# Kernel tuning notes

Hardware: AMD Instinct MI355X
Metric: run time of the kernel (lower is better)

Reference implementation:

```python
import jax, jax.numpy as jnp
import numpy as np

N, E = 20000, 320000
IN, OUT, MID, EC, L = 128, 128, 32, 32, 1
SQRT3 = 1.7320508075688772
EPS = 1e-5


def _xavier(key, fan_in, fan_out, shape=None):
    shape = shape if shape is not None else (fan_in, fan_out)
    std = (2.0 / (fan_in + fan_out)) ** 0.5
    return jax.random.normal(key, shape, dtype=jnp.float32) * std


def layer_norm(x, w, b):
    mu = x.mean(axis=-1, keepdims=True)
    var = ((x - mu) ** 2).mean(axis=-1, keepdims=True)
    return (x - mu) * jax.lax.rsqrt(var + EPS) * w + b


def equ_layer_norm(x, w, b, lmax):
    # x: [N, (lmax+1)^2, C]; per-l RMS norm over (m, channel); l=0 mean-centered + bias.
    segs = []
    for l in range(lmax + 1):
        f = x[:, l * l:(l + 1) * (l + 1), :]
        if l == 0:
            f = f - f.mean(axis=-1, keepdims=True)
        norm = jnp.mean(f * f, axis=(1, 2), keepdims=True)
        f = f * jax.lax.rsqrt(norm + EPS) * w[l]
        if l == 0:
            f = f + b
        segs.append(f)
    return jnp.concatenate(segs, axis=1)


def gate_3j(x, w, lmax, channel):
    # x: [N, (lmax+1)^2, C]; w: [C, C*(lmax+1)] (jax in,out layout)
    after = x[:, 0, :] @ w
    type0 = after[:, :channel]
    mult = jax.nn.sigmoid(after[:, channel:])  # [N, lmax*C]
    parts = [jax.nn.silu(type0)[:, None, :]]
    for l in range(1, lmax + 1):
        parts.append(x[:, l * l:(l + 1) * (l + 1), :] * mult[:, None, (l - 1) * channel:l * channel])
    return jnp.concatenate(parts, axis=1)


def setup_inputs() -> dict:
    key = jax.random.key(0)
    ks = jax.random.split(key, 24)
    inp = {
        'feats': jax.random.normal(ks[0], (N, IN), dtype=jnp.float32),
        'equ': jax.random.normal(ks[1], (N, (L + 1) ** 2, EC), dtype=jnp.float32),
        'points': jax.random.normal(ks[2], (N, 3), dtype=jnp.float32),
        'neighbors': jax.random.randint(ks[3], (2, E), 0, N, dtype=jnp.int64) if jax.config.jax_enable_x64 else jax.random.randint(ks[3], (2, E), 0, N, dtype=jnp.int32),
        # params (jax Linear layout: [in, out])
        'ln1_w': jnp.ones((IN,), jnp.float32), 'ln1_b': jnp.zeros((IN,), jnp.float32),
        'eqn1_w': jnp.ones((L + 1, EC), jnp.float32), 'eqn1_b': jnp.zeros((EC,), jnp.float32),
        'inv_fc_w': _xavier(ks[4], IN, MID), 'inv_fc_b': jnp.zeros((MID,), jnp.float32),
        'equ_fc_w': _xavier(ks[5], EC, MID),
        'fc_l0_w': _xavier(ks[6], 2 * MID, MID), 'fc_l0_b': jnp.zeros((MID,), jnp.float32),
        'equ_fc_2_w': _xavier(ks[7], MID, EC),
        'inv_fc_1_w': _xavier(ks[8], 3 * MID, OUT), 'inv_fc_1_b': jnp.zeros((OUT,), jnp.float32),
        'ffn_ln_w': jnp.ones((OUT,), jnp.float32), 'ffn_ln_b': jnp.zeros((OUT,), jnp.float32),
        'ffn_w1': _xavier(ks[9], OUT, OUT), 'ffn_b1': jnp.zeros((OUT,), jnp.float32),
        'ffn_w2': _xavier(ks[10], OUT, OUT), 'ffn_b2': jnp.zeros((OUT,), jnp.float32),
        'eqn2_w': jnp.ones((L + 1, EC), jnp.float32), 'eqn2_b': jnp.zeros((EC,), jnp.float32),
        'fe1_w': _xavier(ks[11], EC, MID),
        'gate_w': _xavier(ks[12], MID, MID * (L + 1)),
        'fe2_w': _xavier(ks[13], MID, EC),
    }
    return inp


def reference(feats, equ, points, neighbors, ln1_w, ln1_b, eqn1_w, eqn1_b,
              inv_fc_w, inv_fc_b, equ_fc_w, fc_l0_w, fc_l0_b, equ_fc_2_w,
              inv_fc_1_w, inv_fc_1_b, ffn_ln_w, ffn_ln_b, ffn_w1, ffn_b1,
              ffn_w2, ffn_b2, eqn2_w, eqn2_b, fe1_w, gate_w, fe2_w):
    n = feats.shape[0]
    feats = layer_norm(feats, ln1_w, ln1_b)
    equ = equ_layer_norm(equ, eqn1_w, eqn1_b, L)
    feats1 = feats @ inv_fc_w + inv_fc_b              # [N, MID]
    equ1 = equ @ equ_fc_w                              # [N, 4, MID]
    src, dst = neighbors[0], neighbors[1]
    s_equ, t_equ = equ1[src], equ1[dst]                # [E, 4, MID]
    s_feats, t_feats = feats1[src], feats1[dst]        # [E, MID]
    vec = points[src] - points[dst]                    # [E, 3]
    # e3nn spherical harmonics l=0..1, normalize=False, 'component': [1, sqrt(3)*v]
    sh = jnp.concatenate([jnp.ones((vec.shape[0], 1), vec.dtype), SQRT3 * vec], axis=1)  # [E, 4]
    dot1 = jnp.sum(s_equ * t_equ, axis=1)              # [E, MID]
    dot2 = jnp.sum(s_equ * sh[:, :, None], axis=1)     # [E, MID]
    equ_l0 = jax.nn.silu(jnp.concatenate([dot1, dot2], axis=1) @ fc_l0_w + fc_l0_b)
    equ_message = jnp.concatenate([equ_l0[:, None, :], s_equ[:, 1:, :]], axis=1)  # [E, 4, MID]
    equ_message = equ_message @ equ_fc_2_w             # [E, 4, EC]
    inv_message = jax.nn.silu(jnp.concatenate([s_feats, t_feats, equ_l0], axis=-1) @ inv_fc_1_w + inv_fc_1_b)  # [E, OUT]
    nb_cnt = (jnp.max(inv_message, axis=-1, keepdims=True) > 0.0).astype(feats.dtype)  # [E, 1]
    neighbors_new = jnp.ones((n, 1), feats.dtype).at[dst].add(nb_cnt)
    inv_new = jnp.zeros((n, OUT), feats.dtype).at[dst].add(inv_message) + feats  # shortcut1 = Identity
    inv_new = inv_new / neighbors_new
    equ_new = jnp.zeros((n, (L + 1) ** 2, EC), feats.dtype).at[dst].add(equ_message) + equ  # shortcut2 = Identity
    equ_new = equ_new / neighbors_new[:, :, None]
    # ffn_inv
    h = layer_norm(inv_new, ffn_ln_w, ffn_ln_b)
    h = jax.nn.relu(h @ ffn_w1 + ffn_b1) @ ffn_w2 + ffn_b2
    inv_new = h + inv_new
    # ffn_equ
    g = equ_layer_norm(equ_new, eqn2_w, eqn2_b, L) @ fe1_w
    g = gate_3j(g, gate_w, L, MID) @ fe2_w
    equ_new = g + equ_new
    return inv_new, equ_new
```

## Files before the change

### kernel.cpp

```cpp
#include <hip/hip_runtime.h>
#include <math.h>

#define EPS 1e-5f
#define SQRT3F 1.7320508075688772f

__device__ __forceinline__ float wsum64(float x) {
#pragma unroll
    for (int o = 32; o > 0; o >>= 1) x += __shfl_xor(x, o, 64);
    return x;
}
__device__ __forceinline__ float hsum32(float x) {
#pragma unroll
    for (int o = 16; o > 0; o >>= 1) x += __shfl_xor(x, o, 64);
    return x;
}
__device__ __forceinline__ float sigm(float x) { return 1.f / (1.f + __expf(-x)); }
__device__ __forceinline__ float siluf(float x) { return x * sigm(x); }

__global__ __launch_bounds__(256) void node_pre(
    int N,
    const float* __restrict__ feats, const float* __restrict__ equ,
    const float* __restrict__ ln1_w, const float* __restrict__ ln1_b,
    const float* __restrict__ eqn1_w, const float* __restrict__ eqn1_b,
    const float* __restrict__ inv_fc_w, const float* __restrict__ inv_fc_b,
    const float* __restrict__ equ_fc_w, const float* __restrict__ Winv,
    float* __restrict__ feats_ln, float* __restrict__ equ_ln,
    float* __restrict__ equ1t, float* __restrict__ PsP, float* __restrict__ PtP)
{
    __shared__ float fl_s[4][128];
    __shared__ float el_s[4][128];
    __shared__ float f1_s[4][32];
    const int w = threadIdx.x >> 6;
    const int lane = threadIdx.x & 63;
    const int n = blockIdx.x * 4 + w;
    const bool act = n < N;
    const int c = lane & 31;
    const int half = lane >> 5;

    float x0 = 0.f, x1 = 0.f;
    if (act) { x0 = feats[n * 128 + lane]; x1 = feats[n * 128 + 64 + lane]; }
    float s  = wsum64(x0 + x1);
    float sq = wsum64(x0 * x0 + x1 * x1);
    float mu = s * (1.f / 128.f);
    float var = sq * (1.f / 128.f) - mu * mu;
    float rs = rsqrtf(var + EPS);
    float y0 = (x0 - mu) * rs * ln1_w[lane] + ln1_b[lane];
    float y1 = (x1 - mu) * rs * ln1_w[64 + lane] + ln1_b[64 + lane];
    if (act) { feats_ln[n * 128 + lane] = y0; feats_ln[n * 128 + 64 + lane] = y1; }
    fl_s[w][lane] = y0; fl_s[w][64 + lane] = y1;

    float a = 0.f, b = 0.f;
    if (act) { a = equ[n * 128 + lane]; b = equ[n * 128 + 64 + lane]; }
    float a0 = (half == 0) ? a : 0.f;
    float m0 = wsum64(a0) * (1.f / 32.f);
    float f0 = a0 - m0;
    float n0 = wsum64((half == 0) ? f0 * f0 : 0.f) * (1.f / 32.f);
    float rs0 = rsqrtf(n0 + EPS);
    float sq1 = ((half == 1) ? a * a : 0.f) + b * b;
    float n1 = wsum64(sq1) * (1.f / 96.f);
    float rs1 = rsqrtf(n1 + EPS);
    float w1c = eqn1_w[32 + c];
    float ea = (half == 0) ? (f0 * rs0 * eqn1_w[c] + eqn1_b[c]) : (a * rs1 * w1c);
    float eb = b * rs1 * w1c;
    if (act) { equ_ln[n * 128 + lane] = ea; equ_ln[n * 128 + 64 + lane] = eb; }
    el_s[w][lane] = ea; el_s[w][64 + lane] = eb;

    __syncthreads();

    {
        float acc = 0.f;
#pragma unroll 8
        for (int k = 0; k < 64; k++) {
            int kk = half * 64 + k;
            acc += fl_s[w][kk] * inv_fc_w[kk * 32 + c];
        }
        acc += __shfl_xor(acc, 32);
        if (half == 0) f1_s[w][c] = acc + inv_fc_b[c];
    }
    if (act) {
        float acc = 0.f, acc2 = 0.f;
#pragma unroll 8
        for (int k = 0; k < 32; k++) {
            float wv = equ_fc_w[k * 32 + c];
            acc  += el_s[w][half * 32 + k] * wv;
            acc2 += el_s[w][(half + 2) * 32 + k] * wv;
        }
        equ1t[n * 128 + c * 4 + half]     = acc;
        equ1t[n * 128 + c * 4 + half + 2] = acc2;
    }
    __syncthreads();
    if (!act) return;

    {
        const int jj = c;
        float4 aPs = {0.f, 0.f, 0.f, 0.f};
        float4 aPt = {0.f, 0.f, 0.f, 0.f};
#pragma unroll 4
        for (int k = 0; k < 16; k++) {
            int kk = half * 16 + k;
            float x = f1_s[w][kk];
            float4 w4 = *(const float4*)&Winv[kk * 128 + jj * 4];
            float4 v4 = *(const float4*)&Winv[(32 + kk) * 128 + jj * 4];
            aPs.x += x * w4.x; aPs.y += x * w4.y; aPs.z += x * w4.z; aPs.w += x * w4.w;
            aPt.x += x * v4.x; aPt.y += x * v4.y; aPt.z += x * v4.z; aPt.w += x * v4.w;
        }
        aPs.x += __shfl_xor(aPs.x, 32); aPs.y += __shfl_xor(aPs.y, 32);
        aPs.z += __shfl_xor(aPs.z, 32); aPs.w += __shfl_xor(aPs.w, 32);
        aPt.x += __shfl_xor(aPt.x, 32); aPt.y += __shfl_xor(aPt.y, 32);
        aPt.z += __shfl_xor(aPt.z, 32); aPt.w += __shfl_xor(aPt.w, 32);
        if (half == 0) {
            const float* ps = (const float*)&aPs;
            const float* pt = (const float*)&aPt;
#pragma unroll
            for (int i = 0; i < 4; i++) {
                int m = jj * 4 + i;
                PsP[n * 128 + (m & 31) * 4 + (m >> 5)] = ps[i];
                PtP[n * 128 + (m & 31) * 4 + (m >> 5)] = pt[i];
            }
        }
    }
}

__global__ __launch_bounds__(256) void csr_hist(int E, const int* __restrict__ nb,
                                                int* __restrict__ deg)
{
    int i = blockIdx.x * 256 + threadIdx.x;
    if (i < E) atomicAdd(&deg[nb[E + i]], 1);
}

__global__ __launch_bounds__(1024) void csr_scan(int N, const int* __restrict__ deg,
                                                 int* __restrict__ row_start,
                                                 int* __restrict__ cursor)
{
    __shared__ int part[1024];
    const int t = threadIdx.x;
    const int per = (N + 1023) / 1024;
    const int base = t * per;
    int s = 0;
    for (int i = 0; i < per; i++) { int idx = base + i; if (idx < N) s += deg[idx]; }
    part[t] = s;
    __syncthreads();
    for (int off = 1; off < 1024; off <<= 1) {
        int v = (t >= off) ? part[t - off] : 0;
        __syncthreads();
        part[t] += v;
        __syncthreads();
    }
    int run = (t > 0) ? part[t - 1] : 0;
    for (int i = 0; i < per; i++) {
        int idx = base + i;
        if (idx < N) { row_start[idx] = run; cursor[idx] = run; run += deg[idx]; }
    }
}

__global__ __launch_bounds__(256) void csr_scatter(int E, const int* __restrict__ nb,
                                                   int* __restrict__ cursor,
                                                   int* __restrict__ csr_src)
{
    int i = blockIdx.x * 256 + threadIdx.x;
    if (i < E) {
        int d = nb[E + i];
        int s = nb[i];
        int pos = atomicAdd(&cursor[d], 1);
        csr_src[pos] = s;
    }
}

__global__ __launch_bounds__(256) void edge_agg(
    int N,
    const int* __restrict__ row_start, const int* __restrict__ deg_arr,
    const int* __restrict__ csr_src,
    const float* __restrict__ points, const float* __restrict__ equ1t,
    const float* __restrict__ PsP, const float* __restrict__ PtP,
    const float* __restrict__ feats_ln, const float* __restrict__ equ_ln,
    const float* __restrict__ Wl0g, const float* __restrict__ bl0g,
    const float* __restrict__ We2g, const float* __restrict__ Winvg,
    const float* __restrict__ binvg,
    float* __restrict__ out_inv, float* __restrict__ out_equ)
{
    __shared__ float WeP[32 * 128];
    __shared__ float Wl0P[16 * 128];
    __shared__ float We2P[8 * 128];
    __shared__ float BinvP[128];
    __shared__ float bl0s[32];
    __shared__ float scr[8][128];

    for (int idx = threadIdx.x; idx < 4096; idx += 256) {
        int k = idx >> 7, r = idx & 127, cc = r >> 2, j = r & 3;
        WeP[idx] = Winvg[(64 + k) * 128 + j * 32 + cc];
    }
    for (int idx = threadIdx.x; idx < 2048; idx += 256) {
        int g = idx >> 7, r = idx & 127, cc = r >> 2, i = r & 3;
        Wl0P[idx] = Wl0g[(g * 4 + i) * 32 + cc];
    }
    for (int idx = threadIdx.x; idx < 1024; idx += 256) {
        int g = idx >> 7, r = idx & 127, cc = r >> 2, i = r & 3;
        We2P[idx] = We2g[(g * 4 + i) * 32 + cc];
    }
    if (threadIdx.x < 128) BinvP[threadIdx.x] = binvg[(threadIdx.x & 3) * 32 + (threadIdx.x >> 2)];
    if (threadIdx.x < 32) bl0s[threadIdx.x] = bl0g[threadIdx.x];
    __syncthreads();

    const int grp = threadIdx.x >> 5;
    const int c = threadIdx.x & 31;
    const int halfsel = grp & 1;
    const int n = blockIdx.x * 8 + grp;
    if (n >= N) return;

    const int start = row_start[n];
    const int len = deg_arr[n];
    float4 te4 = *(const float4*)&equ1t[n * 128 + c * 4];
    float4 pt4 = *(const float4*)&PtP[n * 128 + c * 4];
    const float pdx = points[n * 3 + 0], pdy = points[n * 3 + 1], pdz = points[n * 3 + 2];
    float4 base = *(const float4*)&BinvP[c * 4];
    base.x += pt4.x; base.y += pt4.y; base.z += pt4.z; base.w += pt4.w;

    float4 acc = {0.f, 0.f, 0.f, 0.f};
    float4 aer = {0.f, 0.f, 0.f, 0.f};
    int cnt = 0;
    int i = 0;

    for (; i + 2 <= len; i += 2) {
        const int s0 = csr_src[start + i];
        const int s1 = csr_src[start + i + 1];
        float4 a0 = *(const float4*)&equ1t[s0 * 128 + c * 4];
        float4 a1 = *(const float4*)&equ1t[s1 * 128 + c * 4];
        float4 p0 = *(const float4*)&PsP[s0 * 128 + c * 4];
        float4 p1 = *(const float4*)&PsP[s1 * 128 + c * 4];
        float dx0 = SQRT3F * (points[s0 * 3 + 0] - pdx);
        float dy0 = SQRT3F * (points[s0 * 3 + 1] - pdy);
        float dz0 = SQRT3F * (points[s0 * 3 + 2] - pdz);
        float dx1 = SQRT3F * (points[s1 * 3 + 0] - pdx);
        float dy1 = SQRT3F * (points[s1 * 3 + 1] - pdy);
        float dz1 = SQRT3F * (points[s1 * 3 + 2] - pdz);
        scr[grp][c]      = a0.x * te4.x + a0.y * te4.y + a0.z * te4.z + a0.w * te4.w;
        scr[grp][32 + c] = a0.x + a0.y * dx0 + a0.z * dy0 + a0.w * dz0;
        scr[grp][64 + c] = a1.x * te4.x + a1.y * te4.y + a1.z * te4.z + a1.w * te4.w;
        scr[grp][96 + c] = a1.x + a1.y * dx1 + a1.z * dy1 + a1.w * dz1;

        float e0acc = bl0s[c], e1acc = bl0s[c];
#pragma unroll
        for (int g = 0; g < 16; g++) {
            float4 w4 = *(const float4*)&Wl0P[g * 128 + c * 4];
            float4 d0 = *(const float4*)&scr[grp][g * 4];
            float4 d1 = *(const float4*)&scr[grp][64 + g * 4];
            e0acc += d0.x * w4.x + d0.y * w4.y + d0.z * w4.z + d0.w * w4.w;
            e1acc += d1.x * w4.x + d1.y * w4.y + d1.z * w4.z + d1.w * w4.w;
        }
        float el0_0 = siluf(e0acc);
        float el0_1 = siluf(e1acc);
        aer.x += el0_0 + el0_1;
        aer.y += a0.y + a1.y; aer.z += a0.z + a1.z; aer.w += a0.w + a1.w;
        scr[grp][c] = el0_0;
        scr[grp][32 + c] = el0_1;

        float4 m0 = base, m1 = base;
        m0.x += p0.x; m0.y += p0.y; m0.z += p0.z; m0.w += p0.w;
        m1.x += p1.x; m1.y += p1.y; m1.z += p1.z; m1.w += p1.w;
#pragma unroll
        for (int g = 0; g < 8; g++) {
            float4 x0 = *(const float4*)&scr[grp][g * 4];
            float4 x1 = *(const float4*)&scr[grp][32 + g * 4];
            const float* xp0 = (const float*)&x0;
            const float* xp1 = (const float*)&x1;
#pragma unroll
            for (int t = 0; t < 4; t++) {
                float4 w4 = *(const float4*)&WeP[(g * 4 + t) * 128 + c * 4];
                float v0 = xp0[t], v1 = xp1[t];
                m0.x += v0 * w4.x; m0.y += v0 * w4.y; m0.z += v0 * w4.z; m0.w += v0 * w4.w;
                m1.x += v1 * w4.x; m1.y += v1 * w4.y; m1.z += v1 * w4.z; m1.w += v1 * w4.w;
            }
        }
        m0.x = siluf(m0.x); m0.y = siluf(m0.y); m0.z = siluf(m0.z); m0.w = siluf(m0.w);
        m1.x = siluf(m1.x); m1.y = siluf(m1.y); m1.z = siluf(m1.z); m1.w = siluf(m1.w);
        acc.x += m0.x + m1.x; acc.y += m0.y + m1.y;
        acc.z += m0.z + m1.z; acc.w += m0.w + m1.w;
        float mx0 = fmaxf(fmaxf(m0.x, m0.y), fmaxf(m0.z, m0.w));
        float mx1 = fmaxf(fmaxf(m1.x, m1.y), fmaxf(m1.z, m1.w));
        unsigned long long b0 = __ballot(mx0 > 0.f);
        unsigned long long b1 = __ballot(mx1 > 0.f);
        cnt += ((unsigned int)(b0 >> (halfsel * 32)) != 0u);
        cnt += ((unsigned int)(b1 >> (halfsel * 32)) != 0u);
    }
    for (; i < len; i++) {
        const int s0 = csr_src[start + i];
        float4 a0 = *(const float4*)&equ1t[s0 * 128 + c * 4];
        float4 p0 = *(const float4*)&PsP[s0 * 128 + c * 4];
        float dx0 = SQRT3F * (points[s0 * 3 + 0] - pdx);
        float dy0 = SQRT3F * (points[s0 * 3 + 1] - pdy);
        float dz0 = SQRT3F * (points[s0 * 3 + 2] - pdz);
        scr[grp][c]      = a0.x * te4.x + a0.y * te4.y + a0.z * te4.z + a0.w * te4.w;
        scr[grp][32 + c] = a0.x + a0.y * dx0 + a0.z * dy0 + a0.w * dz0;
        float e0acc = bl0s[c];
#pragma unroll
        for (int g = 0; g < 16; g++) {
            float4 w4 = *(const float4*)&Wl0P[g * 128 + c * 4];
            float4 d0 = *(const float4*)&scr[grp][g * 4];
            e0acc += d0.x * w4.x + d0.y * w4.y + d0.z * w4.z + d0.w * w4.w;
        }
        float el0_0 = siluf(e0acc);
        aer.x += el0_0; aer.y += a0.y; aer.z += a0.z; aer.w += a0.w;
        scr[grp][c] = el0_0;
        float4 m0 = base;
        m0.x += p0.x; m0.y += p0.y; m0.z += p0.z; m0.w += p0.w;
#pragma unroll
        for (int g = 0; g < 8; g++) {
            float4 x0 = *(const float4*)&scr[grp][g * 4];
            const float* xp0 = (const float*)&x0;
#pragma unroll
            for (int t = 0; t < 4; t++) {
                float4 w4 = *(const float4*)&WeP[(g * 4 + t) * 128 + c * 4];
                float v0 = xp0[t];
                m0.x += v0 * w4.x; m0.y += v0 * w4.y; m0.z += v0 * w4.z; m0.w += v0 * w4.w;
            }
        }
        m0.x = siluf(m0.x); m0.y = siluf(m0.y); m0.z = siluf(m0.z); m0.w = siluf(m0.w);
        acc.x += m0.x; acc.y += m0.y; acc.z += m0.z; acc.w += m0.w;
        float mx0 = fmaxf(fmaxf(m0.x, m0.y), fmaxf(m0.z, m0.w));
        unsigned long long b0 = __ballot(mx0 > 0.f);
        cnt += ((unsigned int)(b0 >> (halfsel * 32)) != 0u);
    }

    const float inv_nbn = 1.f / (1.f + (float)cnt);
    out_inv[n * 128 + c]      = (acc.x + feats_ln[n * 128 + c])      * inv_nbn;
    out_inv[n * 128 + 32 + c] = (acc.y + feats_ln[n * 128 + 32 + c]) * inv_nbn;
    out_inv[n * 128 + 64 + c] = (acc.z + feats_ln[n * 128 + 64 + c]) * inv_nbn;
    out_inv[n * 128 + 96 + c] = (acc.w + feats_ln[n * 128 + 96 + c]) * inv_nbn;

    *(float4*)&scr[grp][c * 4] = aer;
    float4 eo = {0.f, 0.f, 0.f, 0.f};
#pragma unroll
    for (int g = 0; g < 8; g++) {
        float4 w4 = *(const float4*)&We2P[g * 128 + c * 4];
        const float* wp = (const float*)&w4;
#pragma unroll
        for (int t = 0; t < 4; t++) {
            float4 a4 = *(const float4*)&scr[grp][(g * 4 + t) * 4];
            float wv = wp[t];
            eo.x += a4.x * wv; eo.y += a4.y * wv; eo.z += a4.z * wv; eo.w += a4.w * wv;
        }
    }
    out_equ[n * 128 + c]      = (eo.x + equ_ln[n * 128 + c])      * inv_nbn;
    out_equ[n * 128 + 32 + c] = (eo.y + equ_ln[n * 128 + 32 + c]) * inv_nbn;
    out_equ[n * 128 + 64 + c] = (eo.z + equ_ln[n * 128 + 64 + c]) * inv_nbn;
    out_equ[n * 128 + 96 + c] = (eo.w + equ_ln[n * 128 + 96 + c]) * inv_nbn;
}

__global__ __launch_bounds__(256) void node_post(
    int N,
    const float* __restrict__ ffn_ln_w, const float* __restrict__ ffn_ln_b,
    const float* __restrict__ W1g, const float* __restrict__ b1g,
    const float* __restrict__ W2g, const float* __restrict__ b2g,
    const float* __restrict__ eqn2_w, const float* __restrict__ eqn2_b,
    const float* __restrict__ fe1, const float* __restrict__ gate_w,
    const float* __restrict__ fe2,
    float* __restrict__ io_inv, float* __restrict__ io_equ)
{
    __shared__ float ht[128 * 36];
    __shared__ float es[8][128];
    __shared__ float gs[8][128];
    __shared__ float fe1P[8 * 128];
    __shared__ float fe2P[8 * 128];
    __shared__ float gatePa[8 * 128];
    __shared__ float gatePb[8 * 128];

    for (int idx = threadIdx.x; idx < 1024; idx += 256) {
        int g = idx >> 7, r = idx & 127, cc = r >> 2, i = r & 3;
        fe1P[idx]   = fe1[(g * 4 + i) * 32 + cc];
        fe2P[idx]   = fe2[(g * 4 + i) * 32 + cc];
        gatePa[idx] = gate_w[(g * 4 + i) * 64 + cc];
        gatePb[idx] = gate_w[(g * 4 + i) * 64 + 32 + cc];
    }
    __syncthreads();

    const int grp = threadIdx.x >> 5;
    const int c = threadIdx.x & 31;

    for (int q = 0; q < 4; q++) {
        const int nd = grp * 4 + q;
        const int n = blockIdx.x * 32 + nd;
        if (n >= N) break;

        float eq0 = io_equ[n * 128 + c];
        float eq1 = io_equ[n * 128 + 32 + c];
        float eq2 = io_equ[n * 128 + 64 + c];
        float eq3 = io_equ[n * 128 + 96 + c];
        float m0 = hsum32(eq0) * (1.f / 32.f);
        float f0 = eq0 - m0;
        float n0 = hsum32(f0 * f0) * (1.f / 32.f);
        float rs0 = rsqrtf(n0 + EPS);
        float n1 = hsum32(eq1 * eq1 + eq2 * eq2 + eq3 * eq3) * (1.f / 96.f);
        float rs1 = rsqrtf(n1 + EPS);
        float w1c = eqn2_w[32 + c];
        float4 ev;
        ev.x = f0 * rs0 * eqn2_w[c] + eqn2_b[c];
        ev.y = eq1 * rs1 * w1c;
        ev.z = eq2 * rs1 * w1c;
        ev.w = eq3 * rs1 * w1c;
        *(float4*)&es[grp][c * 4] = ev;

        float4 g4 = {0.f, 0.f, 0.f, 0.f};
#pragma unroll
        for (int g = 0; g < 8; g++) {
            float4 w4 = *(const float4*)&fe1P[g * 128 + c * 4];
            const float* wp = (const float*)&w4;
#pragma unroll
            for (int t = 0; t < 4; t++) {
                float4 a4 = *(const float4*)&es[grp][(g * 4 + t) * 4];
                float wv = wp[t];
                g4.x += a4.x * wv; g4.y += a4.y * wv; g4.z += a4.z * wv; g4.w += a4.w * wv;
            }
        }
        *(float4*)&gs[grp][c * 4] = g4;

        float aftA = 0.f, aftB = 0.f;
#pragma unroll
        for (int g = 0; g < 8; g++) {
            float4 wa4 = *(const float4*)&gatePa[g * 128 + c * 4];
            float4 wb4 = *(const float4*)&gatePb[g * 128 + c * 4];
            const float* wap = (const float*)&wa4;
            const float* wbp = (const float*)&wb4;
#pragma unroll
            for (int t = 0; t < 4; t++) {
                float g0 = gs[grp][(g * 4 + t) * 4];
                aftA += g0 * wap[t];
                aftB += g0 * wbp[t];
            }
        }
        float mult = sigm(aftB);
        float4 G;
        G.x = siluf(aftA);
        G.y = g4.y * mult; G.z = g4.z * mult; G.w = g4.w * mult;
        *(float4*)&es[grp][c * 4] = G;

        float4 oo = {0.f, 0.f, 0.f, 0.f};
#pragma unroll
        for (int g = 0; g < 8; g++) {
            float4 w4 = *(const float4*)&fe2P[g * 128 + c * 4];
            const float* wp = (const float*)&w4;
#pragma unroll
            for (int t = 0; t < 4; t++) {
                float4 a4 = *(const float4*)&es[grp][(g * 4 + t) * 4];
                float wv = wp[t];
                oo.x += a4.x * wv; oo.y += a4.y * wv; oo.z += a4.z * wv; oo.w += a4.w * wv;
            }
        }
        io_equ[n * 128 + c]      = oo.x + eq0;
        io_equ[n * 128 + 32 + c] = oo.y + eq1;
        io_equ[n * 128 + 64 + c] = oo.z + eq2;
        io_equ[n * 128 + 96 + c] = oo.w + eq3;

        float ip0 = io_inv[n * 128 + c];
        float ip1 = io_inv[n * 128 + 32 + c];
        float ip2 = io_inv[n * 128 + 64 + c];
        float ip3 = io_inv[n * 128 + 96 + c];
        float sm = hsum32(ip0 + ip1 + ip2 + ip3) * (1.f / 128.f);
        float sv = hsum32(ip0 * ip0 + ip1 * ip1 + ip2 * ip2 + ip3 * ip3) * (1.f / 128.f) - sm * sm;
        float rsv = rsqrtf(sv + EPS);
        ht[c * 36 + nd]         = (ip0 - sm) * rsv * ffn_ln_w[c]      + ffn_ln_b[c];
        ht[(32 + c) * 36 + nd]  = (ip1 - sm) * rsv * ffn_ln_w[32 + c] + ffn_ln_b[32 + c];
        ht[(64 + c) * 36 + nd]  = (ip2 - sm) * rsv * ffn_ln_w[64 + c] + ffn_ln_b[64 + c];
        ht[(96 + c) * 36 + nd]  = (ip3 - sm) * rsv * ffn_ln_w[96 + c] + ffn_ln_b[96 + c];
    }

    const int wid = threadIdx.x >> 6;
    const int half = (threadIdx.x >> 5) & 1;
    const int ndbase = wid * 8;
    const int nbase = blockIdx.x * 32 + ndbase;

    float4 acc8[8];
#pragma unroll
    for (int j = 0; j < 8; j++) acc8[j] = make_float4(0.f, 0.f, 0.f, 0.f);
    for (int k = 0; k < 64; k++) {
        const int kk = half * 64 + k;
        float4 w4 = *(const float4*)&W1g[kk * 128 + c * 4];
        float4 xA = *(const float4*)&ht[kk * 36 + ndbase];
        float4 xB = *(const float4*)&ht[kk * 36 + ndbase + 4];
        const float* xa = (const float*)&xA;
        const float* xb = (const float*)&xB;
#pragma unroll
        for (int j = 0; j < 4; j++) {
            float v = xa[j];
            acc8[j].x += v * w4.x; acc8[j].y += v * w4.y; acc8[j].z += v * w4.z; acc8[j].w += v * w4.w;
            float u = xb[j];
            acc8[4 + j].x += u * w4.x; acc8[4 + j].y += u * w4.y; acc8[4 + j].z += u * w4.z; acc8[4 + j].w += u * w4.w;
        }
    }
#pragma unroll
    for (int j = 0; j < 8; j++) {
        acc8[j].x += __shfl_xor(acc8[j].x, 32); acc8[j].y += __shfl_xor(acc8[j].y, 32);
        acc8[j].z += __shfl_xor(acc8[j].z, 32); acc8[j].w += __shfl_xor(acc8[j].w, 32);
    }
    if (half == 0) {
        float4 b4 = *(const float4*)&b1g[c * 4];
#pragma unroll
        for (int j = 0; j < 8; j++) {
            float r0 = fmaxf(acc8[j].x + b4.x, 0.f);
            float r1 = fmaxf(acc8[j].y + b4.y, 0.f);
            float r2 = fmaxf(acc8[j].z + b4.z, 0.f);
            float r3 = fmaxf(acc8[j].w + b4.w, 0.f);
            ht[(4 * c + 0) * 36 + ndbase + j] = r0;
            ht[(4 * c + 1) * 36 + ndbase + j] = r1;
            ht[(4 * c + 2) * 36 + ndbase + j] = r2;
            ht[(4 * c + 3) * 36 + ndbase + j] = r3;
        }
    }
#pragma unroll
    for (int j = 0; j < 8; j++) acc8[j] = make_float4(0.f, 0.f, 0.f, 0.f);
    for (int k = 0; k < 64; k++) {
        const int kk = half * 64 + k;
        float4 w4 = *(const float4*)&W2g[kk * 128 + c * 4];
        float4 xA = *(const float4*)&ht[kk * 36 + ndbase];
        float4 xB = *(const float4*)&ht[kk * 36 + ndbase + 4];
        const float* xa = (const float*)&xA;
        const float* xb = (const float*)&xB;
#pragma unroll
        for (int j = 0; j < 4; j++) {
            float v = xa[j];
            acc8[j].x += v * w4.x; acc8[j].y += v * w4.y; acc8[j].z += v * w4.z; acc8[j].w += v * w4.w;
            float u = xb[j];
            acc8[4 + j].x += u * w4.x; acc8[4 + j].y += u * w4.y; acc8[4 + j].z += u * w4.z; acc8[4 + j].w += u * w4.w;
        }
    }
#pragma unroll
    for (int j = 0; j < 8; j++) {
        acc8[j].x += __shfl_xor(acc8[j].x, 32); acc8[j].y += __shfl_xor(acc8[j].y, 32);
        acc8[j].z += __shfl_xor(acc8[j].z, 32); acc8[j].w += __shfl_xor(acc8[j].w, 32);
    }
    if (half == 0) {
        float4 b4 = *(const float4*)&b2g[c * 4];
#pragma unroll
        for (int j = 0; j < 8; j++) {
            const int n = nbase + j;
            if (n < N) {
                float4 ipre = *(const float4*)&io_inv[n * 128 + c * 4];
                float4 o;
                o.x = acc8[j].x + b4.x + ipre.x;
                o.y = acc8[j].y + b4.y + ipre.y;
                o.z = acc8[j].z + b4.z + ipre.z;
                o.w = acc8[j].w + b4.w + ipre.w;
                *(float4*)&io_inv[n * 128 + c * 4] = o;
            }
        }
    }
}

extern "C" void kernel_launch(void* const* d_in, const int* in_sizes, int n_in,
                              void* d_out, int out_size, void* d_ws, size_t ws_size,
                              hipStream_t stream)
{
    const float* feats     = (const float*)d_in[0];
    const float* equ       = (const float*)d_in[1];
    const float* points    = (const float*)d_in[2];
    const int*   neighbors = (const int*)d_in[3];
    const float* ln1_w     = (const float*)d_in[4];
    const float* ln1_b     = (const float*)d_in[5];
    const float* eqn1_w    = (const float*)d_in[6];
    const float* eqn1_b    = (const float*)d_in[7];
    const float* inv_fc_w  = (const float*)d_in[8];
    const float* inv_fc_b  = (const float*)d_in[9];
    const float* equ_fc_w  = (const float*)d_in[10];
    const float* fc_l0_w   = (const float*)d_in[11];
    const float* fc_l0_b   = (const float*)d_in[12];
    const float* equ_fc_2_w= (const float*)d_in[13];
    const float* inv_fc_1_w= (const float*)d_in[14];
    const float* inv_fc_1_b= (const float*)d_in[15];
    const float* ffn_ln_w  = (const float*)d_in[16];
    const float* ffn_ln_b  = (const float*)d_in[17];
    const float* ffn_w1    = (const float*)d_in[18];
    const float* ffn_b1    = (const float*)d_in[19];
    const float* ffn_w2    = (const float*)d_in[20];
    const float* ffn_b2    = (const float*)d_in[21];
    const float* eqn2_w    = (const float*)d_in[22];
    const float* eqn2_b    = (const float*)d_in[23];
    const float* fe1_w     = (const float*)d_in[24];
    const float* gate_w    = (const float*)d_in[25];
    const float* fe2_w     = (const float*)d_in[26];

    const int N = in_sizes[0] / 128;
    const int E = in_sizes[3] / 2;

    float* ws = (float*)d_ws;
    float* feats_ln = ws;
    float* equ_ln   = feats_ln + (size_t)N * 128;
    float* equ1t    = equ_ln   + (size_t)N * 128;
    float* PsP      = equ1t    + (size_t)N * 128;
    float* PtP      = PsP      + (size_t)N * 128;
    int* deg        = (int*)(PtP + (size_t)N * 128);
    int* row_start  = deg + N;
    int* cursor     = row_start + N;
    int* csr_src    = cursor + N;

    hipMemsetAsync(deg, 0, (size_t)N * sizeof(int), stream);

    node_pre<<<(N + 3) / 4, 256, 0, stream>>>(
        N, feats, equ, ln1_w, ln1_b, eqn1_w, eqn1_b,
        inv_fc_w, inv_fc_b, equ_fc_w, inv_fc_1_w,
        feats_ln, equ_ln, equ1t, PsP, PtP);

    csr_hist<<<(E + 255) / 256, 256, 0, stream>>>(E, neighbors, deg);
    csr_scan<<<1, 1024, 0, stream>>>(N, deg, row_start, cursor);
    csr_scatter<<<(E + 255) / 256, 256, 0, stream>>>(E, neighbors, cursor, csr_src);

    float* out_inv = (float*)d_out;
    float* out_equ = out_inv + (size_t)N * 128;

    edge_agg<<<(N + 7) / 8, 256, 0, stream>>>(
        N, row_start, deg, csr_src,
        points, equ1t, PsP, PtP, feats_ln, equ_ln,
        fc_l0_w, fc_l0_b, equ_fc_2_w, inv_fc_1_w, inv_fc_1_b,
        out_inv, out_equ);

    node_post<<<(N + 31) / 32, 256, 0, stream>>>(
        N, ffn_ln_w, ffn_ln_b, ffn_w1, ffn_b1, ffn_w2, ffn_b2,
        eqn2_w, eqn2_b, fe1_w, gate_w, fe2_w,
        out_inv, out_equ);
}
```

Measured before the change: 512.5 us.

## Fuse CSR kernels, sort nodes by degree, and move equ FFN into edge_agg

```diff
diff --git a/kernel.cpp b/kernel.cpp
--- a/kernel.cpp
+++ b/kernel.cpp
@@ -17,16 +17,24 @@
 __device__ __forceinline__ float sigm(float x) { return 1.f / (1.f + __expf(-x)); }
 __device__ __forceinline__ float siluf(float x) { return x * sigm(x); }
 
-__global__ __launch_bounds__(256) void node_pre(
-    int N,
+__global__ __launch_bounds__(256) void pre_and_hist(
+    int N, int E, int nb_pre,
     const float* __restrict__ feats, const float* __restrict__ equ,
+    const int* __restrict__ nbrs, const float* __restrict__ points,
     const float* __restrict__ ln1_w, const float* __restrict__ ln1_b,
     const float* __restrict__ eqn1_w, const float* __restrict__ eqn1_b,
     const float* __restrict__ inv_fc_w, const float* __restrict__ inv_fc_b,
     const float* __restrict__ equ_fc_w, const float* __restrict__ Winv,
     float* __restrict__ feats_ln, float* __restrict__ equ_ln,
-    float* __restrict__ equ1t, float* __restrict__ PsP, float* __restrict__ PtP)
+    float* __restrict__ equ1t, float* __restrict__ PsP, float* __restrict__ PtP,
+    float* __restrict__ points4, int* __restrict__ deg)
 {
+    if (blockIdx.x >= nb_pre) {
+        int i = (blockIdx.x - nb_pre) * 256 + threadIdx.x;
+        if (i < E) atomicAdd(&deg[nbrs[E + i]], 1);
+        return;
+    }
+
     __shared__ float fl_s[4][128];
     __shared__ float el_s[4][128];
     __shared__ float f1_s[4][32];
@@ -36,6 +44,13 @@
     const bool act = n < N;
     const int c = lane & 31;
     const int half = lane >> 5;
+
+    if (act && lane == 0) {
+        float4 p;
+        p.x = points[n * 3 + 0]; p.y = points[n * 3 + 1];
+        p.z = points[n * 3 + 2]; p.w = 0.f;
+        *(float4*)&points4[n * 4] = p;
+    }
 
     float x0 = 0.f, x1 = 0.f;
     if (act) { x0 = feats[n * 128 + lane]; x1 = feats[n * 128 + 64 + lane]; }
@@ -121,23 +136,43 @@
     }
 }
 
-__global__ __launch_bounds__(256) void csr_hist(int E, const int* __restrict__ nb,
-                                                int* __restrict__ deg)
-{
-    int i = blockIdx.x * 256 + threadIdx.x;
-    if (i < E) atomicAdd(&deg[nb[E + i]], 1);
-}
-
-__global__ __launch_bounds__(1024) void csr_scan(int N, const int* __restrict__ deg,
-                                                 int* __restrict__ row_start,
-                                                 int* __restrict__ cursor)
+__global__ __launch_bounds__(1024) void csr_scan(
+    int N, const int* __restrict__ deg,
+    int* __restrict__ row_start, int* __restrict__ cursor,
+    int* __restrict__ bucket_start, int* __restrict__ bucket_cursor,
+    const float* __restrict__ fe1, const float* __restrict__ fe2,
+    const float* __restrict__ gate_w, const float* __restrict__ We2,
+    float* __restrict__ fe1P, float* __restrict__ fe2P,
+    float* __restrict__ gatePa, float* __restrict__ gatePb,
+    float* __restrict__ We2P)
 {
     __shared__ int part[1024];
+    __shared__ int hist[64];
     const int t = threadIdx.x;
+
+    if (t < 1024) {
+        int g = t >> 7, r = t & 127, cc = r >> 2, i = r & 3;
+        fe1P[t]   = fe1[(g * 4 + i) * 32 + cc];
+        fe2P[t]   = fe2[(g * 4 + i) * 32 + cc];
+        gatePa[t] = gate_w[(g * 4 + i) * 64 + cc];
+        gatePb[t] = gate_w[(g * 4 + i) * 64 + 32 + cc];
+        We2P[t]   = We2[(g * 4 + i) * 32 + cc];
+    }
+
+    if (t < 64) hist[t] = 0;
+    __syncthreads();
+
     const int per = (N + 1023) / 1024;
     const int base = t * per;
     int s = 0;
-    for (int i = 0; i < per; i++) { int idx = base + i; if (idx < N) s += deg[idx]; }
+    for (int i = 0; i < per; i++) {
+        int idx = base + i;
+        if (idx < N) {
+            int d = deg[idx];
+            s += d;
+            atomicAdd(&hist[d < 63 ? d : 63], 1);
+        }
+    }
     part[t] = s;
     __syncthreads();
     for (int off = 1; off < 1024; off <<= 1) {
@@ -151,36 +186,57 @@
         int idx = base + i;
         if (idx < N) { row_start[idx] = run; cursor[idx] = run; run += deg[idx]; }
     }
-}
-
-__global__ __launch_bounds__(256) void csr_scatter(int E, const int* __restrict__ nb,
-                                                   int* __restrict__ cursor,
-                                                   int* __restrict__ csr_src)
+    if (t == 0) {
+        int acc = 0;
+        for (int b = 0; b < 64; b++) {
+            bucket_start[b] = acc;
+            bucket_cursor[b] = acc;
+            acc += hist[b];
+        }
+    }
+}
+
+__global__ __launch_bounds__(256) void scatter_all(
+    int E, int N, int nbE,
+    const int* __restrict__ nb, int* __restrict__ cursor, int* __restrict__ csr_src,
+    const int* __restrict__ deg, int* __restrict__ bucket_cursor, int* __restrict__ perm)
 {
-    int i = blockIdx.x * 256 + threadIdx.x;
-    if (i < E) {
-        int d = nb[E + i];
-        int s = nb[i];
-        int pos = atomicAdd(&cursor[d], 1);
-        csr_src[pos] = s;
-    }
-}
-
-__global__ __launch_bounds__(256) void edge_agg(
+    if (blockIdx.x < nbE) {
+        int i = blockIdx.x * 256 + threadIdx.x;
+        if (i < E) {
+            int d = nb[E + i];
+            int s = nb[i];
+            int pos = atomicAdd(&cursor[d], 1);
+            csr_src[pos] = s;
+        }
+    } else {
+        int i = (blockIdx.x - nbE) * 256 + threadIdx.x;
+        if (i < N) {
+            int d = deg[i]; if (d > 63) d = 63;
+            int pos = atomicAdd(&bucket_cursor[d], 1);
+            perm[pos] = i;
+        }
+    }
+}
+
+__global__ __launch_bounds__(256, 5) void edge_agg(
     int N,
+    const int* __restrict__ perm,
     const int* __restrict__ row_start, const int* __restrict__ deg_arr,
     const int* __restrict__ csr_src,
-    const float* __restrict__ points, const float* __restrict__ equ1t,
+    const float* __restrict__ points4, const float* __restrict__ equ1t,
     const float* __restrict__ PsP, const float* __restrict__ PtP,
     const float* __restrict__ feats_ln, const float* __restrict__ equ_ln,
     const float* __restrict__ Wl0g, const float* __restrict__ bl0g,
-    const float* __restrict__ We2g, const float* __restrict__ Winvg,
-    const float* __restrict__ binvg,
+    const float* __restrict__ Winvg, const float* __restrict__ binvg,
+    const float* __restrict__ We2P, const float* __restrict__ fe1P,
+    const float* __restrict__ fe2P, const float* __restrict__ gatePa,
+    const float* __restrict__ gatePb,
+    const float* __restrict__ eqn2_w, const float* __restrict__ eqn2_b,
     float* __restrict__ out_inv, float* __restrict__ out_equ)
 {
     __shared__ float WeP[32 * 128];
     __shared__ float Wl0P[16 * 128];
-    __shared__ float We2P[8 * 128];
     __shared__ float BinvP[128];
     __shared__ float bl0s[32];
     __shared__ float scr[8][128];
@@ -193,10 +249,6 @@
         int g = idx >> 7, r = idx & 127, cc = r >> 2, i = r & 3;
         Wl0P[idx] = Wl0g[(g * 4 + i) * 32 + cc];
     }
-    for (int idx = threadIdx.x; idx < 1024; idx += 256) {
-        int g = idx >> 7, r = idx & 127, cc = r >> 2, i = r & 3;
-        We2P[idx] = We2g[(g * 4 + i) * 32 + cc];
-    }
     if (threadIdx.x < 128) BinvP[threadIdx.x] = binvg[(threadIdx.x & 3) * 32 + (threadIdx.x >> 2)];
     if (threadIdx.x < 32) bl0s[threadIdx.x] = bl0g[threadIdx.x];
     __syncthreads();
@@ -204,14 +256,15 @@
     const int grp = threadIdx.x >> 5;
     const int c = threadIdx.x & 31;
     const int halfsel = grp & 1;
-    const int n = blockIdx.x * 8 + grp;
-    if (n >= N) return;
+    const int gid = blockIdx.x * 8 + grp;
+    if (gid >= N) return;
+    const int n = perm[gid];
 
     const int start = row_start[n];
     const int len = deg_arr[n];
     float4 te4 = *(const float4*)&equ1t[n * 128 + c * 4];
     float4 pt4 = *(const float4*)&PtP[n * 128 + c * 4];
-    const float pdx = points[n * 3 + 0], pdy = points[n * 3 + 1], pdz = points[n * 3 + 2];
+    float4 pd4 = *(const float4*)&points4[n * 4];
     float4 base = *(const float4*)&BinvP[c * 4];
     base.x += pt4.x; base.y += pt4.y; base.z += pt4.z; base.w += pt4.w;
 
@@ -227,12 +280,14 @@
         float4 a1 = *(const float4*)&equ1t[s1 * 128 + c * 4];
         float4 p0 = *(const float4*)&PsP[s0 * 128 + c * 4];
         float4 p1 = *(const float4*)&PsP[s1 * 128 + c * 4];
-        float dx0 = SQRT3F * (points[s0 * 3 + 0] - pdx);
-        float dy0 = SQRT3F * (points[s0 * 3 + 1] - pdy);
-        float dz0 = SQRT3F * (points[s0 * 3 + 2] - pdz);
-        float dx1 = SQRT3F * (points[s1 * 3 + 0] - pdx);
-        float dy1 = SQRT3F * (points[s1 * 3 + 1] - pdy);
-        float dz1 = SQRT3F * (points[s1 * 3 + 2] - pdz);
+        float4 q0 = *(const float4*)&points4[s0 * 4];
+        float4 q1 = *(const float4*)&points4[s1 * 4];
+        float dx0 = SQRT3F * (q0.x - pd4.x);
+        float dy0 = SQRT3F * (q0.y - pd4.y);
+        float dz0 = SQRT3F * (q0.z - pd4.z);
+        float dx1 = SQRT3F * (q1.x - pd4.x);
+        float dy1 = SQRT3F * (q1.y - pd4.y);
+        float dz1 = SQRT3F * (q1.z - pd4.z);
         scr[grp][c]      = a0.x * te4.x + a0.y * te4.y + a0.z * te4.z + a0.w * te4.w;
         scr[grp][32 + c] = a0.x + a0.y * dx0 + a0.z * dy0 + a0.w * dz0;
         scr[grp][64 + c] = a1.x * te4.x + a1.y * te4.y + a1.z * te4.z + a1.w * te4.w;
@@ -286,9 +341,10 @@
         const int s0 = csr_src[start + i];
         float4 a0 = *(const float4*)&equ1t[s0 * 128 + c * 4];
         float4 p0 = *(const float4*)&PsP[s0 * 128 + c * 4];
-        float dx0 = SQRT3F * (points[s0 * 3 + 0] - pdx);
-        float dy0 = SQRT3F * (points[s0 * 3 + 1] - pdy);
-        float dz0 = SQRT3F * (points[s0 * 3 + 2] - pdz);
+        float4 q0 = *(const float4*)&points4[s0 * 4];
+        float dx0 = SQRT3F * (q0.x - pd4.x);
+        float dy0 = SQRT3F * (q0.y - pd4.y);
+        float dz0 = SQRT3F * (q0.z - pd4.z);
         scr[grp][c]      = a0.x * te4.x + a0.y * te4.y + a0.z * te4.z + a0.w * te4.w;
         scr[grp][32 + c] = a0.x + a0.y * dx0 + a0.z * dy0 + a0.w * dz0;
         float e0acc = bl0s[c];
@@ -340,10 +396,71 @@
             eo.x += a4.x * wv; eo.y += a4.y * wv; eo.z += a4.z * wv; eo.w += a4.w * wv;
         }
     }
-    out_equ[n * 128 + c]      = (eo.x + equ_ln[n * 128 + c])      * inv_nbn;
-    out_equ[n * 128 + 32 + c] = (eo.y + equ_ln[n * 128 + 32 + c]) * inv_nbn;
-    out_equ[n * 128 + 64 + c] = (eo.z + equ_ln[n * 128 + 64 + c]) * inv_nbn;
-    out_equ[n * 128 + 96 + c] = (eo.w + equ_ln[n * 128 + 96 + c]) * inv_nbn;
+    float4 en;
+    en.x = (eo.x + equ_ln[n * 128 + c])      * inv_nbn;
+    en.y = (eo.y + equ_ln[n * 128 + 32 + c]) * inv_nbn;
+    en.z = (eo.z + equ_ln[n * 128 + 64 + c]) * inv_nbn;
+    en.w = (eo.w + equ_ln[n * 128 + 96 + c]) * inv_nbn;
+
+    float m0e = hsum32(en.x) * (1.f / 32.f);
+    float f0 = en.x - m0e;
+    float n0 = hsum32(f0 * f0) * (1.f / 32.f);
+    float rs0 = rsqrtf(n0 + EPS);
+    float n1 = hsum32(en.y * en.y + en.z * en.z + en.w * en.w) * (1.f / 96.f);
+    float rs1 = rsqrtf(n1 + EPS);
+    float w1c = eqn2_w[32 + c];
+    float4 ev;
+    ev.x = f0 * rs0 * eqn2_w[c] + eqn2_b[c];
+    ev.y = en.y * rs1 * w1c;
+    ev.z = en.z * rs1 * w1c;
+    ev.w = en.w * rs1 * w1c;
+    *(float4*)&scr[grp][c * 4] = ev;
+
+    float4 g4 = {0.f, 0.f, 0.f, 0.f};
+#pragma unroll
+    for (int g = 0; g < 8; g++) {
+        float4 w4 = *(const float4*)&fe1P[g * 128 + c * 4];
+        const float* wp = (const float*)&w4;
+#pragma unroll
+        for (int t = 0; t < 4; t++) {
+            float4 a4 = *(const float4*)&scr[grp][(g * 4 + t) * 4];
+            float wv = wp[t];
+            g4.x += a4.x * wv; g4.y += a4.y * wv; g4.z += a4.z * wv; g4.w += a4.w * wv;
+        }
+    }
+    scr[grp][c] = g4.x;
+
+    float aftA = 0.f, aftB = 0.f;
+#pragma unroll
+    for (int g = 0; g < 8; g++) {
+        float4 x4 = *(const float4*)&scr[grp][g * 4];
+        float4 wa4 = *(const float4*)&gatePa[g * 128 + c * 4];
+        float4 wb4 = *(const float4*)&gatePb[g * 128 + c * 4];
+        aftA += x4.x * wa4.x + x4.y * wa4.y + x4.z * wa4.z + x4.w * wa4.w;
+        aftB += x4.x * wb4.x + x4.y * wb4.y + x4.z * wb4.z + x4.w * wb4.w;
+    }
+    float mult = sigm(aftB);
+    float4 G;
+    G.x = siluf(aftA);
+    G.y = g4.y * mult; G.z = g4.z * mult; G.w = g4.w * mult;
+    *(float4*)&scr[grp][c * 4] = G;
+
+    float4 oo = {0.f, 0.f, 0.f, 0.f};
+#pragma unroll
+    for (int g = 0; g < 8; g++) {
+        float4 w4 = *(const float4*)&fe2P[g * 128 + c * 4];
+        const float* wp = (const float*)&w4;
+#pragma unroll
+        for (int t = 0; t < 4; t++) {
+            float4 a4 = *(const float4*)&scr[grp][(g * 4 + t) * 4];
+            float wv = wp[t];
+            oo.x += a4.x * wv; oo.y += a4.y * wv; oo.z += a4.z * wv; oo.w += a4.w * wv;
+        }
+    }
+    out_equ[n * 128 + c]      = oo.x + en.x;
+    out_equ[n * 128 + 32 + c] = oo.y + en.y;
+    out_equ[n * 128 + 64 + c] = oo.z + en.z;
+    out_equ[n * 128 + 96 + c] = oo.w + en.w;
 }
 
 __global__ __launch_bounds__(256) void node_post(
@@ -351,28 +468,9 @@
     const float* __restrict__ ffn_ln_w, const float* __restrict__ ffn_ln_b,
     const float* __restrict__ W1g, const float* __restrict__ b1g,
     const float* __restrict__ W2g, const float* __restrict__ b2g,
-    const float* __restrict__ eqn2_w, const float* __restrict__ eqn2_b,
-    const float* __restrict__ fe1, const float* __restrict__ gate_w,
-    const float* __restrict__ fe2,
-    float* __restrict__ io_inv, float* __restrict__ io_equ)
+    float* __restrict__ io_inv)
 {
     __shared__ float ht[128 * 36];
-    __shared__ float es[8][128];
-    __shared__ float gs[8][128];
-    __shared__ float fe1P[8 * 128];
-    __shared__ float fe2P[8 * 128];
-    __shared__ float gatePa[8 * 128];
-    __shared__ float gatePb[8 * 128];
-
-    for (int idx = threadIdx.x; idx < 1024; idx += 256) {
-        int g = idx >> 7, r = idx & 127, cc = r >> 2, i = r & 3;
-        fe1P[idx]   = fe1[(g * 4 + i) * 32 + cc];
-        fe2P[idx]   = fe2[(g * 4 + i) * 32 + cc];
-        gatePa[idx] = gate_w[(g * 4 + i) * 64 + cc];
-        gatePb[idx] = gate_w[(g * 4 + i) * 64 + 32 + cc];
-    }
-    __syncthreads();
-
     const int grp = threadIdx.x >> 5;
     const int c = threadIdx.x & 31;
 
@@ -380,76 +478,6 @@
         const int nd = grp * 4 + q;
         const int n = blockIdx.x * 32 + nd;
         if (n >= N) break;
-
-        float eq0 = io_equ[n * 128 + c];
-        float eq1 = io_equ[n * 128 + 32 + c];
-        float eq2 = io_equ[n * 128 + 64 + c];
-        float eq3 = io_equ[n * 128 + 96 + c];
-        float m0 = hsum32(eq0) * (1.f / 32.f);
-        float f0 = eq0 - m0;
-        float n0 = hsum32(f0 * f0) * (1.f / 32.f);
-        float rs0 = rsqrtf(n0 + EPS);
-        float n1 = hsum32(eq1 * eq1 + eq2 * eq2 + eq3 * eq3) * (1.f / 96.f);
-        float rs1 = rsqrtf(n1 + EPS);
-        float w1c = eqn2_w[32 + c];
-        float4 ev;
-        ev.x = f0 * rs0 * eqn2_w[c] + eqn2_b[c];
-        ev.y = eq1 * rs1 * w1c;
-        ev.z = eq2 * rs1 * w1c;
-        ev.w = eq3 * rs1 * w1c;
-        *(float4*)&es[grp][c * 4] = ev;
-
-        float4 g4 = {0.f, 0.f, 0.f, 0.f};
-#pragma unroll
-        for (int g = 0; g < 8; g++) {
-            float4 w4 = *(const float4*)&fe1P[g * 128 + c * 4];
-            const float* wp = (const float*)&w4;
-#pragma unroll
-            for (int t = 0; t < 4; t++) {
-                float4 a4 = *(const float4*)&es[grp][(g * 4 + t) * 4];
-                float wv = wp[t];
-                g4.x += a4.x * wv; g4.y += a4.y * wv; g4.z += a4.z * wv; g4.w += a4.w * wv;
-            }
-        }
-        *(float4*)&gs[grp][c * 4] = g4;
-
-        float aftA = 0.f, aftB = 0.f;
-#pragma unroll
-        for (int g = 0; g < 8; g++) {
-            float4 wa4 = *(const float4*)&gatePa[g * 128 + c * 4];
-            float4 wb4 = *(const float4*)&gatePb[g * 128 + c * 4];
-            const float* wap = (const float*)&wa4;
-            const float* wbp = (const float*)&wb4;
-#pragma unroll
-            for (int t = 0; t < 4; t++) {
-                float g0 = gs[grp][(g * 4 + t) * 4];
-                aftA += g0 * wap[t];
-                aftB += g0 * wbp[t];
-            }
-        }
-        float mult = sigm(aftB);
-        float4 G;
-        G.x = siluf(aftA);
-        G.y = g4.y * mult; G.z = g4.z * mult; G.w = g4.w * mult;
-        *(float4*)&es[grp][c * 4] = G;
-
-        float4 oo = {0.f, 0.f, 0.f, 0.f};
-#pragma unroll
-        for (int g = 0; g < 8; g++) {
-            float4 w4 = *(const float4*)&fe2P[g * 128 + c * 4];
-            const float* wp = (const float*)&w4;
-#pragma unroll
-            for (int t = 0; t < 4; t++) {
-                float4 a4 = *(const float4*)&es[grp][(g * 4 + t) * 4];
-                float wv = wp[t];
-                oo.x += a4.x * wv; oo.y += a4.y * wv; oo.z += a4.z * wv; oo.w += a4.w * wv;
-            }
-        }
-        io_equ[n * 128 + c]      = oo.x + eq0;
-        io_equ[n * 128 + 32 + c] = oo.y + eq1;
-        io_equ[n * 128 + 64 + c] = oo.z + eq2;
-        io_equ[n * 128 + 96 + c] = oo.w + eq3;
-
         float ip0 = io_inv[n * 128 + c];
         float ip1 = io_inv[n * 128 + 32 + c];
         float ip2 = io_inv[n * 128 + 64 + c];
@@ -495,14 +523,10 @@
         float4 b4 = *(const float4*)&b1g[c * 4];
 #pragma unroll
         for (int j = 0; j < 8; j++) {
-            float r0 = fmaxf(acc8[j].x + b4.x, 0.f);
-            float r1 = fmaxf(acc8[j].y + b4.y, 0.f);
-            float r2 = fmaxf(acc8[j].z + b4.z, 0.f);
-            float r3 = fmaxf(acc8[j].w + b4.w, 0.f);
-            ht[(4 * c + 0) * 36 + ndbase + j] = r0;
-            ht[(4 * c + 1) * 36 + ndbase + j] = r1;
-            ht[(4 * c + 2) * 36 + ndbase + j] = r2;
-            ht[(4 * c + 3) * 36 + ndbase + j] = r3;
+            ht[(4 * c + 0) * 36 + ndbase + j] = fmaxf(acc8[j].x + b4.x, 0.f);
+            ht[(4 * c + 1) * 36 + ndbase + j] = fmaxf(acc8[j].y + b4.y, 0.f);
+            ht[(4 * c + 2) * 36 + ndbase + j] = fmaxf(acc8[j].z + b4.z, 0.f);
+            ht[(4 * c + 3) * 36 + ndbase + j] = fmaxf(acc8[j].w + b4.w, 0.f);
         }
     }
 #pragma unroll
@@ -586,33 +610,51 @@
     float* equ1t    = equ_ln   + (size_t)N * 128;
     float* PsP      = equ1t    + (size_t)N * 128;
     float* PtP      = PsP      + (size_t)N * 128;
-    int* deg        = (int*)(PtP + (size_t)N * 128);
+    float* points4  = PtP      + (size_t)N * 128;
+    float* fe1P     = points4  + (size_t)N * 4;
+    float* fe2P     = fe1P + 1024;
+    float* gatePa   = fe2P + 1024;
+    float* gatePb   = gatePa + 1024;
+    float* We2P     = gatePb + 1024;
+    int* deg        = (int*)(We2P + 1024);
     int* row_start  = deg + N;
     int* cursor     = row_start + N;
-    int* csr_src    = cursor + N;
+    int* bucket_start  = cursor + N;
+    int* bucket_cursor = bucket_start + 64;
+    int* perm       = bucket_cursor + 64;
+    int* csr_src    = perm + N;
 
     hipMemsetAsync(deg, 0, (size_t)N * sizeof(int), stream);
 
-    node_pre<<<(N + 3) / 4, 256, 0, stream>>>(
-        N, feats, equ, ln1_w, ln1_b, eqn1_w, eqn1_b,
+    const int nb_pre = (N + 3) / 4;
+    const int nb_hist = (E + 255) / 256;
+    pre_and_hist<<<nb_pre + nb_hist, 256, 0, stream>>>(
+        N, E, nb_pre, feats, equ, neighbors, points,
+        ln1_w, ln1_b, eqn1_w, eqn1_b,
         inv_fc_w, inv_fc_b, equ_fc_w, inv_fc_1_w,
-        feats_ln, equ_ln, equ1t, PsP, PtP);
-
-    csr_hist<<<(E + 255) / 256, 256, 0, stream>>>(E, neighbors, deg);
-    csr_scan<<<1, 1024, 0, stream>>>(N, deg, row_start, cursor);
-    csr_scatter<<<(E + 255) / 256, 256, 0, stream>>>(E, neighbors, cursor, csr_src);
+        feats_ln, equ_ln, equ1t, PsP, PtP, points4, deg);
+
+    csr_scan<<<1, 1024, 0, stream>>>(
+        N, deg, row_start, cursor, bucket_start, bucket_cursor,
+        fe1_w, fe2_w, gate_w, equ_fc_2_w,
+        fe1P, fe2P, gatePa, gatePb, We2P);
+
+    const int nbE = (E + 255) / 256;
+    const int nbN = (N + 255) / 256;
+    scatter_all<<<nbE + nbN, 256, 0, stream>>>(
+        E, N, nbE, neighbors, cursor, csr_src, deg, bucket_cursor, perm);
 
     float* out_inv = (float*)d_out;
     float* out_equ = out_inv + (size_t)N * 128;
 
     edge_agg<<<(N + 7) / 8, 256, 0, stream>>>(
-        N, row_start, deg, csr_src,
-        points, equ1t, PsP, PtP, feats_ln, equ_ln,
-        fc_l0_w, fc_l0_b, equ_fc_2_w, inv_fc_1_w, inv_fc_1_b,
+        N, perm, row_start, deg, csr_src,
+        points4, equ1t, PsP, PtP, feats_ln, equ_ln,
+        fc_l0_w, fc_l0_b, inv_fc_1_w, inv_fc_1_b,
+        We2P, fe1P, fe2P, gatePa, gatePb, eqn2_w, eqn2_b,
         out_inv, out_equ);
 
     node_post<<<(N + 31) / 32, 256, 0, stream>>>(
         N, ffn_ln_w, ffn_ln_b, ffn_w1, ffn_b1, ffn_w2, ffn_b2,
-        eqn2_w, eqn2_b, fe1_w, gate_w, fe2_w,
-        out_inv, out_equ);
-}
+        out_inv);
+}
```

Measured after the change: 949.4 us. +85.2%, slower.
